# Performance work log

Hardware: AMD Instinct MI355X
Metric: run time of the kernel (lower is better)

The kernel has to match this reference:

```python
import jax, jax.numpy as jnp
import numpy as np

N = 40000      # nodes
E = 640000     # directed edges (avg degree 16)
IN_DIM = 64
HID = 64
OUT = 128
EPS_LN = 1e-5
EPS_BN = 1e-5
NEG_SLOPE = 0.2  # PyG GATConv default


def setup_inputs() -> dict:
    key = jax.random.key(0)
    ks = jax.random.split(key, 40)
    s = 0.05
    d = {}
    d["x"] = jax.random.normal(ks[0], (N, IN_DIM), jnp.float32)
    d["edge_index"] = jax.random.randint(ks[1], (2, E), 0, N, jnp.int32)
    d["pos"] = jax.random.normal(ks[2], (N, 3), jnp.float32)
    # GAT layer 1: in=64, out=64, heads=4 (concat)
    d["W1"] = jax.random.normal(ks[3], (4 * HID, IN_DIM), jnp.float32) * s
    d["a_s1"] = jax.random.normal(ks[4], (4, HID), jnp.float32) * s
    d["a_d1"] = jax.random.normal(ks[5], (4, HID), jnp.float32) * s
    d["bg1"] = jnp.zeros((4 * HID,), jnp.float32)
    d["ln1_g"] = jnp.ones((4 * HID,), jnp.float32)
    d["ln1_b"] = jnp.zeros((4 * HID,), jnp.float32)
    # GAT layer 2: in=256, out=64, heads=2 (concat)
    d["W2"] = jax.random.normal(ks[6], (2 * HID, 4 * HID), jnp.float32) * s
    d["a_s2"] = jax.random.normal(ks[7], (2, HID), jnp.float32) * s
    d["a_d2"] = jax.random.normal(ks[8], (2, HID), jnp.float32) * s
    d["bg2"] = jnp.zeros((2 * HID,), jnp.float32)
    d["ln2_g"] = jnp.ones((2 * HID,), jnp.float32)
    d["ln2_b"] = jnp.zeros((2 * HID,), jnp.float32)
    # GAT layer 3: in=128, out=128, heads=1
    d["W3"] = jax.random.normal(ks[9], (OUT, 2 * HID), jnp.float32) * s
    d["a_s3"] = jax.random.normal(ks[10], (1, OUT), jnp.float32) * s
    d["a_d3"] = jax.random.normal(ks[11], (1, OUT), jnp.float32) * s
    d["bg3"] = jnp.zeros((OUT,), jnp.float32)
    # pointnet: Conv1d(3,64,1) -> BN -> ReLU -> Conv1d(64,128,1) -> BN -> ReLU -> Conv1d(128,128,1)
    d["pw1"] = jax.random.normal(ks[12], (64, 3), jnp.float32) * s
    d["pb1"] = jnp.zeros((64,), jnp.float32)
    d["bn1_g"] = jnp.ones((64,), jnp.float32)
    d["bn1_b"] = jnp.zeros((64,), jnp.float32)
    d["pw2"] = jax.random.normal(ks[13], (128, 64), jnp.float32) * s
    d["pb2"] = jnp.zeros((128,), jnp.float32)
    d["bn2_g"] = jnp.ones((128,), jnp.float32)
    d["bn2_b"] = jnp.zeros((128,), jnp.float32)
    d["pw3"] = jax.random.normal(ks[14], (OUT, 128), jnp.float32) * s
    d["pb3"] = jnp.zeros((OUT,), jnp.float32)
    # fusion Linear(2*OUT, OUT)
    d["fw"] = jax.random.normal(ks[15], (OUT, 2 * OUT), jnp.float32) * s
    d["fb"] = jnp.zeros((OUT,), jnp.float32)
    return d


def _gat(x, W, a_s, a_d, b, src, dst, n):
    """PyG-style GATConv (concat=True, eval mode). x:[n,Fin], W:[H*C,Fin], a_*:[H,C]."""
    H, C = a_s.shape
    h = (x @ W.T).reshape(n, H, C)                       # [n,H,C]
    e_src = jnp.sum(h * a_s[None], -1)                   # [n,H]
    e_dst = jnp.sum(h * a_d[None], -1)                   # [n,H]
    e = jax.nn.leaky_relu(e_src[src] + e_dst[dst], NEG_SLOPE)   # [E,H]
    emax = jax.ops.segment_max(e, dst, num_segments=n)   # segment softmax over dst
    ex = jnp.exp(e - emax[dst])
    den = jax.ops.segment_sum(ex, dst, num_segments=n)
    alpha = ex / (den[dst] + 1e-16)                      # [E,H]
    out = jax.ops.segment_sum(alpha[:, :, None] * h[src], dst, num_segments=n)  # [n,H,C]
    return out.reshape(n, H * C) + b


def _ln(x, g, b):
    mu = jnp.mean(x, -1, keepdims=True)
    var = jnp.var(x, -1, keepdims=True)
    return (x - mu) * jax.lax.rsqrt(var + EPS_LN) * g + b


def _bn_eval(x, g, b):
    # eval-mode BatchNorm with freshly-initialized running stats (mean=0, var=1)
    return x * (g * jax.lax.rsqrt(jnp.float32(1.0 + EPS_BN))) + b


def reference(x, edge_index, pos, W1, a_s1, a_d1, bg1, ln1_g, ln1_b,
              W2, a_s2, a_d2, bg2, ln2_g, ln2_b, W3, a_s3, a_d3, bg3,
              pw1, pb1, bn1_g, bn1_b, pw2, pb2, bn2_g, bn2_b, pw3, pb3, fw, fb):
    n = x.shape[0]
    loops = jnp.arange(n, dtype=edge_index.dtype)        # PyG add_self_loops=True
    src = jnp.concatenate([edge_index[0], loops])
    dst = jnp.concatenate([edge_index[1], loops])

    x1 = jax.nn.relu(_ln(_gat(x, W1, a_s1, a_d1, bg1, src, dst, n), ln1_g, ln1_b))
    x2 = jax.nn.relu(_ln(_gat(x1, W2, a_s2, a_d2, bg2, src, dst, n), ln2_g, ln2_b))
    x3 = _gat(x2, W3, a_s3, a_d3, bg3, src, dst, n)      # [n,OUT]

    # pointnet: 1x1 conv1d == per-node linear
    p = jax.nn.relu(_bn_eval(pos @ pw1.T + pb1, bn1_g, bn1_b))
    p = jax.nn.relu(_bn_eval(p @ pw2.T + pb2, bn2_g, bn2_b))
    pos_features = p @ pw3.T + pb3                       # [n,OUT]

    combined = jnp.concatenate([x3, pos_features], -1)
    output = combined @ fw.T + fb
    return (output, x3, pos_features)
```

## Files before the change

kernel.cpp:

```cpp
#include <hip/hip_runtime.h>
#include <cstddef>

#define NNODES 40000
#define NEDGES 640000
#define NETOT  (NNODES + NEDGES)
#define ELLW   96
#define NCAST  30720
#define NBUCK  313
#define SEGCAP 8192
#define ABLOCKS 84
#define CBLOCKS 30

typedef unsigned short u16;
typedef unsigned int   u32;
using v2f = __attribute__((ext_vector_type(2))) float;

__device__ inline float wave_sum(float v) {
#pragma unroll
    for (int o = 32; o > 0; o >>= 1) v += __shfl_xor(v, o);
    return v;
}
__device__ inline u16 f2bf(float f) {
    u32 u = __float_as_uint(f);
    return (u16)((u + 0x7fffu + ((u >> 16) & 1u)) >> 16);
}

__global__ void build_a_kernel(const int* __restrict__ ei, u32* __restrict__ bcnt,
                               u32* __restrict__ seg,
                               const float* __restrict__ W1, const float* __restrict__ as1,
                               const float* __restrict__ ad1, float* __restrict__ vbuf,
                               const float* s0, u16* d0, int n0, const float* s1, u16* d1, int n1,
                               const float* s2, u16* d2, int n2, const float* s3, u16* d3, int n3,
                               const float* s4, u16* d4, int n4, const float* s5, u16* d5, int n5) {
    int tid = threadIdx.x;
    int blk = blockIdx.x;
    if (blk >= ABLOCKS) {
        if (blk < ABLOCKS + CBLOCKS) {
            int i = (blk - ABLOCKS) * 1024 + tid;
            const float* s; u16* d;
            if      (i < n0) { s = s0; d = d0; }
            else if ((i -= n0) < n1) { s = s1; d = d1; }
            else if ((i -= n1) < n2) { s = s2; d = d2; }
            else if ((i -= n2) < n3) { s = s3; d = d3; }
            else if ((i -= n3) < n4) { s = s4; d = d4; }
            else if ((i -= n4) < n5) { s = s5; d = d5; }
            else return;
            float4 v = ((const float4*)s)[i];
            ushort4 o; o.x = f2bf(v.x); o.y = f2bf(v.y); o.z = f2bf(v.z); o.w = f2bf(v.w);
            ((ushort4*)d)[i] = o;
        } else if (tid < 256) {
            int h = tid >> 6, k = tid & 63;
            float ss = 0.f, dd = 0.f;
            for (int c = 0; c < 64; c++) {
                float w = W1[(h * 64 + c) * 64 + k];
                ss += as1[h * 64 + c] * w;
                dd += ad1[h * 64 + c] * w;
            }
            vbuf[tid] = ss;
            vbuf[256 + tid] = dd;
        }
        return;
    }
    __shared__ u32 hist[NBUCK], hbase[NBUCK];
    for (int i = tid; i < NBUCK; i += 1024) hist[i] = 0;
    __syncthreads();
    u32 pk[8], loc[8]; int bj[8];
    int g0 = blk * 8192;
#pragma unroll
    for (int j = 0; j < 8; j++) {
        int g = g0 + j * 1024 + tid;
        bj[j] = -1;
        if (g < NETOT) {
            int src, dst;
            if (g < NEDGES) { src = ei[g]; dst = ei[NEDGES + g]; }
            else            { src = g - NEDGES; dst = src; }
            int b = dst >> 7;
            pk[j] = ((u32)dst << 16) | (u32)src;
            bj[j] = b;
            loc[j] = atomicAdd(&hist[b], 1u);
        }
    }
    __syncthreads();
    for (int i = tid; i < NBUCK; i += 1024) {
        u32 c = hist[i];
        hbase[i] = c ? atomicAdd(&bcnt[i], c) : 0u;
    }
    __syncthreads();
#pragma unroll
    for (int j = 0; j < 8; j++) {
        if (bj[j] >= 0) {
            u32 pos = hbase[bj[j]] + loc[j];
            if (pos < SEGCAP) seg[(size_t)bj[j] * SEGCAP + pos] = pk[j];
        }
    }
}

__global__ void build_b_kernel(const u32* __restrict__ seg, const u32* __restrict__ bcnt,
                               int* __restrict__ cnt, u16* __restrict__ srcs16,
                               int2* __restrict__ ovbuf) {
    __shared__ u32 lcnt[128];
    int tid = threadIdx.x;
    int b = blockIdx.x;
    int base = b << 7;
    if (tid < 128) lcnt[tid] = 0;
    __syncthreads();
    u32 m = bcnt[b]; if (m > SEGCAP) m = SEGCAP;
    const u32* sp = seg + (size_t)b * SEGCAP;
    for (u32 e = tid; e < m; e += 256) {
        u32 pkv = sp[e];
        u32 dst = pkv >> 16, src = pkv & 0xffffu;
        u32 p = atomicAdd(&lcnt[dst - (u32)base], 1u);
        if (p < ELLW) srcs16[dst * ELLW + p] = (u16)src;
        else {
            int q = atomicAdd(&cnt[NNODES], 1);
            ovbuf[q] = make_int2((int)dst, (int)src);
        }
    }
    __syncthreads();
    if (tid < 128 && base + tid < NNODES) cnt[base + tid] = (int)lcnt[tid];
}

__global__ void esed1_kernel(const float* __restrict__ x, const float* __restrict__ vbuf,
                             float* __restrict__ es, float* __restrict__ ed,
                             u16* __restrict__ xc) {
    __shared__ float vl[512];
    int tid = threadIdx.x;
    vl[tid] = vbuf[tid];
    vl[tid + 256] = vbuf[tid + 256];
    __syncthreads();
    int lane = tid & 63, wave = tid >> 6;
    int i = lane >> 2, q = lane & 3;
    int node = blockIdx.x * 64 + wave * 16 + i;
    const float* xp = x + (size_t)node * 64 + q * 16;
    float xr[16];
    *(float4*)&xr[0]  = ((const float4*)xp)[0];
    *(float4*)&xr[4]  = ((const float4*)xp)[1];
    *(float4*)&xr[8]  = ((const float4*)xp)[2];
    *(float4*)&xr[12] = ((const float4*)xp)[3];
    float p[8];
#pragma unroll
    for (int h = 0; h < 8; h++) {
        float s = 0.f;
#pragma unroll
        for (int j = 0; j < 16; j++) s += xr[j] * vl[h * 64 + q * 16 + j];
        p[h] = s;
    }
#pragma unroll
    for (int h = 0; h < 8; h++) {
        p[h] += __shfl_xor(p[h], 1);
        p[h] += __shfl_xor(p[h], 2);
    }
    es[node * 4 + q] = p[q];
    ed[node * 4 + q] = p[4 + q];
    u16* cp = xc + (size_t)node * 64 + q * 16;
#pragma unroll
    for (int j = 0; j < 16; j += 4) {
        ushort4 o; o.x = f2bf(xr[j]); o.y = f2bf(xr[j + 1]);
        o.z = f2bf(xr[j + 2]); o.w = f2bf(xr[j + 3]);
        *(ushort4*)(cp + j) = o;
    }
}

__global__ void gat_agg_kernel(const u16* __restrict__ xc,
                               const float* __restrict__ es, const float* __restrict__ ed,
                               const int* __restrict__ cnt, const u16* __restrict__ srcs16,
                               const int2* __restrict__ ovbuf,
                               u16* __restrict__ agg, int n) {
    __shared__ float wbuf[4][4][100];
    __shared__ u32   sbuf[4][ELLW];
    int wave = threadIdx.x >> 6;
    int wid = (blockIdx.x * blockDim.x + threadIdx.x) >> 6;
    int lane = threadIdx.x & 63;
    if (wid >= n) return;

    int degt = cnt[wid];
    int mainc = degt < ELLW ? degt : ELLW;
    int padt = (mainc + 7) & ~7;
    const u16* sp = srcs16 + (size_t)wid * ELLW;

    const int h = lane & 3;
    const int esub = lane >> 2;
    float edh = ed[(size_t)wid * 4 + h];

    float den = 0.f;
    for (int i0 = 0; i0 < padt; i0 += 16) {
        int e = i0 + esub;
        if (e < padt) {
            float w = 0.f; u32 off = 0;
            if (e < mainc) {
                int s = sp[e];
                off = (u32)s << 7;
                float v = es[(size_t)s * 4 + h] + edh;
                v = v > 0.f ? v : 0.2f * v;
                w = __expf(v);
            }
            wbuf[wave][h][e] = w;
            if (h == 0) sbuf[wave][e] = off;
            den += w;
        }
    }
    int ovn = 0;
    if (degt > ELLW) {
        ovn = cnt[n];
        for (int j = esub; j < ovn; j += 16) {
            int2 t = ovbuf[j];
            if (t.x == wid) {
                float v = es[(size_t)t.y * 4 + h] + edh;
                v = v > 0.f ? v : 0.2f * v;
                den += __expf(v);
            }
        }
    }
#pragma unroll
    for (int o = 4; o < 64; o <<= 1) den += __shfl_xor(den, o);
    float inv = 1.f / (den + 1e-16f);

    const int e2 = lane >> 5, f16 = lane & 31;
    const char* hp = (const char*)xc + f16 * 4;
    v2f a0 = {0.f, 0.f}, a1 = {0.f, 0.f}, a2 = {0.f, 0.f}, a3 = {0.f, 0.f};
    for (int eb = 0; eb < padt; eb += 8) {
        u32 of[4]; u32 g[4];
        float w0[4], w1[4], w2[4], w3[4];
#pragma unroll
        for (int k = 0; k < 4; k++) of[k] = sbuf[wave][eb + 2 * k + e2];
#pragma unroll
        for (int k = 0; k < 4; k++) g[k] = *(const u32*)(hp + of[k]);
#pragma unroll
        for (int k = 0; k < 4; k++) {
            int e = eb + 2 * k + e2;
            w0[k] = wbuf[wave][0][e]; w1[k] = wbuf[wave][1][e];
            w2[k] = wbuf[wave][2][e]; w3[k] = wbuf[wave][3][e];
        }
#pragma unroll
        for (int k = 0; k < 4; k++) {
            v2f hx;
            hx.x = __uint_as_float(g[k] << 16);
            hx.y = __uint_as_float(g[k] & 0xffff0000u);
            a0 += v2f{w0[k], w0[k]} * hx;
            a1 += v2f{w1[k], w1[k]} * hx;
            a2 += v2f{w2[k], w2[k]} * hx;
            a3 += v2f{w3[k], w3[k]} * hx;
        }
    }
    if (degt > ELLW) {
        for (int j = 0; j < ovn; j++) {
            int2 t = ovbuf[j];
            if (t.x != wid) continue;
            float wh[4];
#pragma unroll
            for (int hh = 0; hh < 4; hh++) {
                float v = es[(size_t)t.y * 4 + hh] + __shfl(edh, hh);
                v = v > 0.f ? v : 0.2f * v;
                wh[hh] = __expf(v);
            }
            if (lane < 32) {
                u32 g = *(const u32*)(hp + ((u32)t.y << 7));
                v2f hx;
                hx.x = __uint_as_float(g << 16);
                hx.y = __uint_as_float(g & 0xffff0000u);
                a0 += v2f{wh[0], wh[0]} * hx;
                a1 += v2f{wh[1], wh[1]} * hx;
                a2 += v2f{wh[2], wh[2]} * hx;
                a3 += v2f{wh[3], wh[3]} * hx;
            }
        }
    }
    a0.x += __shfl_xor(a0.x, 32); a0.y += __shfl_xor(a0.y, 32);
    a1.x += __shfl_xor(a1.x, 32); a1.y += __shfl_xor(a1.y, 32);
    a2.x += __shfl_xor(a2.x, 32); a2.y += __shfl_xor(a2.y, 32);
    a3.x += __shfl_xor(a3.x, 32); a3.y += __shfl_xor(a3.y, 32);
    float iv[4];
#pragma unroll
    for (int hh = 0; hh < 4; hh++) iv[hh] = __shfl(inv, hh);
    if (lane < 32) {
        u32* op = (u32*)agg + (size_t)wid * 128 + f16;
        op[0]  = ((u32)f2bf(a0.y * iv[0]) << 16) | f2bf(a0.x * iv[0]);
        op[32] = ((u32)f2bf(a1.y * iv[1]) << 16) | f2bf(a1.x * iv[1]);
        op[64] = ((u32)f2bf(a2.y * iv[2]) << 16) | f2bf(a2.x * iv[2]);
        op[96] = ((u32)f2bf(a3.y * iv[3]) << 16) | f2bf(a3.x * iv[3]);
    }
}

__global__ void w1ln_kernel(const u16* __restrict__ agg, const u16* __restrict__ B,
                            const float* __restrict__ bias,
                            const float* __restrict__ lng, const float* __restrict__ lnb,
                            u16* __restrict__ xb, int M) {
    using bfrag = __attribute__((ext_vector_type(8))) short;
    using ffrag = __attribute__((ext_vector_type(4))) float;
    int wave = threadIdx.x >> 6, lane = threadIdx.x & 63;
    int lm = lane & 15, kg = (lane >> 4) * 8;
    int rowblk = blockIdx.x * 64 + wave * 16;
    ffrag acc[16] = {};
#pragma unroll
    for (int hh = 0; hh < 4; hh++) {
#pragma unroll
        for (int k0 = 0; k0 < 64; k0 += 32) {
            bfrag af = *(const bfrag*)(agg + (size_t)(rowblk + lm) * 256 + hh * 64 + kg + k0);
#pragma unroll
            for (int tt = 0; tt < 4; tt++) {
                int t = hh * 4 + tt;
                bfrag bf = *(const bfrag*)(B + (size_t)(hh * 64 + tt * 16 + lm) * 64 + kg + k0);
                acc[t] = __builtin_amdgcn_mfma_f32_16x16x32_bf16(af, bf, acc[t], 0, 0, 0);
            }
        }
    }
    int orow = rowblk + (lane >> 4) * 4;
    float bi[16], gg[16], bb[16];
#pragma unroll
    for (int t = 0; t < 16; t++) {
        int col = t * 16 + lm;
        bi[t] = bias[col]; gg[t] = lng[col]; bb[t] = lnb[col];
    }
#pragma unroll
    for (int r = 0; r < 4; r++) {
        float pv[16];
        float s1 = 0.f, s2 = 0.f;
#pragma unroll
        for (int t = 0; t < 16; t++) {
            float v = acc[t][r] + bi[t];
            pv[t] = v; s1 += v; s2 += v * v;
        }
#pragma unroll
        for (int o = 1; o < 16; o <<= 1) { s1 += __shfl_xor(s1, o); s2 += __shfl_xor(s2, o); }
        float mu = s1 / 256.f;
        float var = s2 / 256.f - mu * mu;
        float rstd = rsqrtf(var + 1e-5f);
#pragma unroll
        for (int t = 0; t < 16; t++) {
            float v = (pv[t] - mu) * rstd * gg[t] + bb[t];
            v = v > 0.f ? v : 0.f;
            xb[(size_t)(orow + r) * 256 + t * 16 + lm] = f2bf(v);
        }
    }
}

template <int H, int C, bool AF32>
__global__ void gemm_scores_kernel(const void* __restrict__ Aptr, const u16* __restrict__ B,
                                   u16* __restrict__ Cout,
                                   const float* __restrict__ as, const float* __restrict__ ad,
                                   float* __restrict__ es, float* __restrict__ ed,
                                   int M, int Nn, int K) {
    constexpr int HT = 128 / C;
    using bfrag = __attribute__((ext_vector_type(8))) short;
    using ffrag = __attribute__((ext_vector_type(4))) float;
    int wave = threadIdx.x >> 6, lane = threadIdx.x & 63;
    int lm = lane & 15, kg = (lane >> 4) * 8;
    int rowblk = blockIdx.x * 64 + wave * 16;
    int n0 = blockIdx.y * 128;
    const u16* Bp = B + (size_t)(n0 + lm) * K + kg;
    ffrag acc[8] = {};
    for (int k0 = 0; k0 < K; k0 += 32) {
        bfrag af;
        if constexpr (AF32) {
            const float* ap = (const float*)Aptr + (size_t)(rowblk + lm) * K + kg + k0;
            float4 a0 = *(const float4*)ap;
            float4 a1 = *(const float4*)(ap + 4);
            af[0] = (short)f2bf(a0.x); af[1] = (short)f2bf(a0.y);
            af[2] = (short)f2bf(a0.z); af[3] = (short)f2bf(a0.w);
            af[4] = (short)f2bf(a1.x); af[5] = (short)f2bf(a1.y);
            af[6] = (short)f2bf(a1.z); af[7] = (short)f2bf(a1.w);
        } else {
            af = *(const bfrag*)((const u16*)Aptr + (size_t)(rowblk + lm) * K + kg + k0);
        }
#pragma unroll
        for (int t = 0; t < 8; t++) {
            bfrag bf = *(const bfrag*)(Bp + (size_t)t * 16 * K + k0);
            acc[t] = __builtin_amdgcn_mfma_f32_16x16x32_bf16(af, bf, acc[t], 0, 0, 0);
        }
    }
    int orow = rowblk + (lane >> 4) * 4;
    float asv[8], adv[8];
#pragma unroll
    for (int t = 0; t < 8; t++) {
        int fcol = n0 + t * 16 + lm;
        asv[t] = as[fcol]; adv[t] = ad[fcol];
    }
    float ps[4][HT] = {}, pd[4][HT] = {};
#pragma unroll
    for (int t = 0; t < 8; t++) {
        const int hh = t / (C / 16);
#pragma unroll
        for (int r = 0; r < 4; r++) {
            float v = acc[t][r];
            ps[r][hh] += v * asv[t];
            pd[r][hh] += v * adv[t];
            Cout[(size_t)(orow + r) * Nn + n0 + t * 16 + lm] = f2bf(v);
        }
    }
    int hb = blockIdx.y * HT;
#pragma unroll
    for (int r = 0; r < 4; r++)
#pragma unroll
        for (int hh = 0; hh < HT; hh++) {
            float s = ps[r][hh], d = pd[r][hh];
#pragma unroll
            for (int o = 1; o < 16; o <<= 1) { s += __shfl_xor(s, o); d += __shfl_xor(d, o); }
            if (lm == 0) {
                es[(size_t)(orow + r) * H + hb + hh] = s;
                ed[(size_t)(orow + r) * H + hb + hh] = d;
            }
        }
}

template <int H, int C, bool LNRELU>
__global__ void gat_fused_kernel(const u16* __restrict__ hmat,
                                 const float* __restrict__ es, const float* __restrict__ ed,
                                 const int* __restrict__ cnt, const u16* __restrict__ srcs16,
                                 const int2* __restrict__ ovbuf,
                                 const float* __restrict__ bias,
                                 const float* __restrict__ lng, const float* __restrict__ lnb,
                                 void* __restrict__ out, int n) {
    constexpr int HC = H * C;
    constexpr int VPT = HC / 64;
    constexpr int SH = (HC == 256) ? 9 : 8;
    constexpr int EPW = 64 / H;
    constexpr int HSH = (H == 4) ? 2 : ((H == 2) ? 1 : 0);
    __shared__ float wbuf[4][H][100];
    __shared__ int   sbuf[4][ELLW];
    int wave = threadIdx.x >> 6;
    int wid = (blockIdx.x * blockDim.x + threadIdx.x) >> 6;
    int lane = threadIdx.x & 63;
    if (wid >= n) return;

    int degt = cnt[wid];
    int mainc = degt < ELLW ? degt : ELLW;
    int pad = (mainc + 7) & ~7;
    const u16* sp = srcs16 + (size_t)wid * ELLW;

    const int h = lane & (H - 1);
    const int esub = lane >> HSH;
    float edh = ed[(size_t)wid * H + h];

    float den = 0.f;
    for (int i0 = 0; i0 < pad; i0 += EPW) {
        int e = i0 + esub;
        if (e < pad) {
            float w = 0.f;
            int soff = 0;
            if (e < mainc) {
                int s = sp[e];
                soff = s << SH;
                float v = es[(size_t)s * H + h] + edh;
                v = v > 0.f ? v : 0.2f * v;
                w = __expf(v);
            }
            wbuf[wave][h][e] = w;
            if (h == 0) sbuf[wave][e] = soff;
            den += w;
        }
    }
    int ovn = 0;
    if (degt > ELLW) {
        ovn = cnt[n];
        for (int j = esub; j < ovn; j += EPW) {
            int2 t = ovbuf[j];
            if (t.x == wid) {
                float v = es[(size_t)t.y * H + h] + edh;
                v = v > 0.f ? v : 0.2f * v;
                den += __expf(v);
            }
        }
    }
#pragma unroll
    for (int o = H; o < 64; o <<= 1) den += __shfl_xor(den, o);
    float inv = 1.f / (den + 1e-16f);

    const int myhead = (lane * VPT) / C;
    const float invh = __shfl(inv, myhead);
    const int loff = lane * (VPT * 2);
    v2f a01 = {0.f, 0.f}, a23 = {0.f, 0.f};

    for (int e = 0; e < pad; e += 8) {
        int4   o0 = *(const int4*)&sbuf[wave][e];
        int4   o1 = *(const int4*)&sbuf[wave][e + 4];
        float4 w0 = *(const float4*)&wbuf[wave][myhead][e];
        float4 w1 = *(const float4*)&wbuf[wave][myhead][e + 4];
        int   oo[8] = {o0.x, o0.y, o0.z, o0.w, o1.x, o1.y, o1.z, o1.w};
        float ww[8] = {w0.x, w0.y, w0.z, w0.w, w1.x, w1.y, w1.z, w1.w};
        if constexpr (VPT == 4) {
            uint2 gg[8];
#pragma unroll
            for (int u = 0; u < 8; u++)
                gg[u] = *(const uint2*)((const char*)hmat + (size_t)(u32)oo[u] + loff);
#pragma unroll
            for (int u = 0; u < 8; u++) {
                v2f wv = {ww[u], ww[u]};
                v2f h01, h23;
                h01.x = __uint_as_float(gg[u].x << 16);
                h01.y = __uint_as_float(gg[u].x & 0xffff0000u);
                h23.x = __uint_as_float(gg[u].y << 16);
                h23.y = __uint_as_float(gg[u].y & 0xffff0000u);
                a01 += wv * h01;
                a23 += wv * h23;
            }
        } else {
            u32 gg[8];
#pragma unroll
            for (int u = 0; u < 8; u++)
                gg[u] = *(const u32*)((const char*)hmat + (size_t)(u32)oo[u] + loff);
#pragma unroll
            for (int u = 0; u < 8; u++) {
                v2f wv = {ww[u], ww[u]};
                v2f h01;
                h01.x = __uint_as_float(gg[u] << 16);
                h01.y = __uint_as_float(gg[u] & 0xffff0000u);
                a01 += wv * h01;
            }
        }
    }
    if (degt > ELLW) {
        const float edm = __shfl(edh, myhead);
        for (int j = 0; j < ovn; j++) {
            int2 t = ovbuf[j];
            if (t.x != wid) continue;
            float v = es[(size_t)t.y * H + myhead] + edm;
            v = v > 0.f ? v : 0.2f * v;
            float w = __expf(v);
            v2f wv = {w, w};
            if constexpr (VPT == 4) {
                uint2 g = *(const uint2*)((const char*)hmat + ((size_t)t.y << SH) + loff);
                v2f h01, h23;
                h01.x = __uint_as_float(g.x << 16);
                h01.y = __uint_as_float(g.x & 0xffff0000u);
                h23.x = __uint_as_float(g.y << 16);
                h23.y = __uint_as_float(g.y & 0xffff0000u);
                a01 += wv * h01;
                a23 += wv * h23;
            } else {
                u32 g = *(const u32*)((const char*)hmat + ((size_t)t.y << SH) + loff);
                v2f h01;
                h01.x = __uint_as_float(g << 16);
                h01.y = __uint_as_float(g & 0xffff0000u);
                a01 += wv * h01;
            }
        }
    }
    {
        v2f iv = {invh, invh};
        a01 *= iv;
        a23 *= iv;
    }

    int fbase = lane * VPT;
    float y[VPT];
    y[0] = a01.x + bias[fbase + 0];
    y[1] = a01.y + bias[fbase + 1];
    if constexpr (VPT == 4) {
        y[2] = a23.x + bias[fbase + 2];
        y[3] = a23.y + bias[fbase + 3];
    }

    if constexpr (LNRELU) {
        float s1 = 0.f, s2 = 0.f;
#pragma unroll
        for (int j = 0; j < VPT; j++) { s1 += y[j]; s2 += y[j] * y[j]; }
        s1 = wave_sum(s1);
        s2 = wave_sum(s2);
        float mu = s1 / (float)HC;
        float var = s2 / (float)HC - mu * mu;
        float rstd = rsqrtf(var + 1e-5f);
#pragma unroll
        for (int j = 0; j < VPT; j++) {
            float v = (y[j] - mu) * rstd * lng[fbase + j] + lnb[fbase + j];
            y[j] = v > 0.f ? v : 0.f;
        }
        u16* op = (u16*)out + (size_t)wid * HC + fbase;
        if constexpr (VPT == 4) {
            ushort4 o; o.x = f2bf(y[0]); o.y = f2bf(y[1]); o.z = f2bf(y[2]); o.w = f2bf(y[3]);
            *(ushort4*)op = o;
        } else {
            ushort2 o; o.x = f2bf(y[0]); o.y = f2bf(y[1]);
            *(ushort2*)op = o;
        }
    } else {
        float* op = (float*)out + (size_t)wid * HC + fbase;
        if constexpr (VPT == 4) *(float4*)op = make_float4(y[0], y[1], y[2], y[3]);
        else                    *(float2*)op = make_float2(y[0], y[1]);
    }
}

__global__ void gemm_pn12_kernel(const float* __restrict__ pos,
                                 const float* __restrict__ pw1, const float* __restrict__ pb1,
                                 const float* __restrict__ bn1g, const float* __restrict__ bn1b,
                                 const u16* __restrict__ B, u16* __restrict__ Cout,
                                 const float* __restrict__ pb2,
                                 const float* __restrict__ bn2g, const float* __restrict__ bn2b,
                                 int M) {
    const int Nn = 128, K = 64;
    using bfrag = __attribute__((ext_vector_type(8))) short;
    using ffrag = __attribute__((ext_vector_type(4))) float;
    int wave = threadIdx.x >> 6, lane = threadIdx.x & 63;
    int lm = lane & 15, kg = (lane >> 4) * 8;
    int rowblk = blockIdx.x * 64 + wave * 16;
    int row = rowblk + lm;
    float p0 = pos[row * 3 + 0], p1 = pos[row * 3 + 1], p2 = pos[row * 3 + 2];
    const u16* Bp = B + (size_t)lm * K + kg;
    const float bnscale = rsqrtf(1.0f + 1e-5f);
    ffrag acc[8] = {};
#pragma unroll
    for (int k0 = 0; k0 < K; k0 += 32) {
        bfrag af;
#pragma unroll
        for (int j = 0; j < 8; j++) {
            int k = kg + k0 + j;
            float v = p0 * pw1[k * 3 + 0] + p1 * pw1[k * 3 + 1] + p2 * pw1[k * 3 + 2] + pb1[k];
            v = v * (bn1g[k] * bnscale) + bn1b[k];
            v = v > 0.f ? v : 0.f;
            af[j] = (short)f2bf(v);
        }
#pragma unroll
        for (int t = 0; t < 8; t++) {
            bfrag bf = *(const bfrag*)(Bp + (size_t)t * 16 * K + k0);
            acc[t] = __builtin_amdgcn_mfma_f32_16x16x32_bf16(af, bf, acc[t], 0, 0, 0);
        }
    }
    int orow = rowblk + (lane >> 4) * 4;
#pragma unroll
    for (int t = 0; t < 8; t++) {
        int col = t * 16 + lm;
        float bi = pb2[col], g = bn2g[col] * bnscale, bb = bn2b[col];
#pragma unroll
        for (int r = 0; r < 4; r++) {
            float v = (acc[t][r] + bi) * g + bb;
            v = v > 0.f ? v : 0.f;
            Cout[(size_t)(orow + r) * Nn + col] = f2bf(v);
        }
    }
}

__global__ void gemm_pw3cat_kernel(const u16* __restrict__ p2, const u16* __restrict__ Bpw3,
                                   const float* __restrict__ pb3, float* __restrict__ pf,
                                   const float* __restrict__ x3, const u16* __restrict__ Bfw,
                                   const float* __restrict__ fb, float* __restrict__ outp,
                                   int M) {
    using bfrag = __attribute__((ext_vector_type(8))) short;
    using ffrag = __attribute__((ext_vector_type(4))) float;
    __shared__ float pft[64][132];
    int wave = threadIdx.x >> 6, lane = threadIdx.x & 63;
    int lm = lane & 15, kg = (lane >> 4) * 8;
    int rowblk = blockIdx.x * 64 + wave * 16;

    {
        const u16* Ap = p2 + (size_t)(rowblk + lm) * 128 + kg;
        const u16* Bp = Bpw3 + (size_t)lm * 128 + kg;
        ffrag acc[8] = {};
#pragma unroll
        for (int k0 = 0; k0 < 128; k0 += 32) {
            bfrag af = *(const bfrag*)(Ap + k0);
#pragma unroll
            for (int t = 0; t < 8; t++) {
                bfrag bf = *(const bfrag*)(Bp + (size_t)t * 16 * 128 + k0);
                acc[t] = __builtin_amdgcn_mfma_f32_16x16x32_bf16(af, bf, acc[t], 0, 0, 0);
            }
        }
        int orow = rowblk + (lane >> 4) * 4;
        int lrow = wave * 16 + (lane >> 4) * 4;
#pragma unroll
        for (int t = 0; t < 8; t++) {
            int col = t * 16 + lm;
            float bi = pb3[col];
#pragma unroll
            for (int r = 0; r < 4; r++) {
                float v = acc[t][r] + bi;
                pf[(size_t)(orow + r) * 128 + col] = v;
                pft[lrow + r][col] = v;
            }
        }
    }
    __syncthreads();

    {
        const u16* Bp = Bfw + (size_t)lm * 256 + kg;
        ffrag acc[8] = {};
        int row = rowblk + lm, lrow = wave * 16 + lm;
#pragma unroll
        for (int k0 = 0; k0 < 256; k0 += 32) {
            bfrag af;
            if (k0 < 128) {
                const float* ap = x3 + (size_t)row * 128 + kg + k0;
                float4 a0 = *(const float4*)ap;
                float4 a1 = *(const float4*)(ap + 4);
                af[0] = (short)f2bf(a0.x); af[1] = (short)f2bf(a0.y);
                af[2] = (short)f2bf(a0.z); af[3] = (short)f2bf(a0.w);
                af[4] = (short)f2bf(a1.x); af[5] = (short)f2bf(a1.y);
                af[6] = (short)f2bf(a1.z); af[7] = (short)f2bf(a1.w);
            } else {
                const float* ap = &pft[lrow][kg + k0 - 128];
                float4 a0 = *(const float4*)ap;
                float4 a1 = *(const float4*)(ap + 4);
                af[0] = (short)f2bf(a0.x); af[1] = (short)f2bf(a0.y);
                af[2] = (short)f2bf(a0.z); af[3] = (short)f2bf(a0.w);
                af[4] = (short)f2bf(a1.x); af[5] = (short)f2bf(a1.y);
                af[6] = (short)f2bf(a1.z); af[7] = (short)f2bf(a1.w);
            }
#pragma unroll
            for (int t = 0; t < 8; t++) {
                bfrag bf = *(const bfrag*)(Bp + (size_t)t * 16 * 256 + k0);
                acc[t] = __builtin_amdgcn_mfma_f32_16x16x32_bf16(af, bf, acc[t], 0, 0, 0);
            }
        }
        int orow = rowblk + (lane >> 4) * 4;
#pragma unroll
        for (int t = 0; t < 8; t++) {
            int col = t * 16 + lm;
            float bi = fb[col];
#pragma unroll
            for (int r = 0; r < 4; r++)
                outp[(size_t)(orow + r) * 128 + col] = acc[t][r] + bi;
        }
    }
}

extern "C" void kernel_launch(void* const* d_in, const int* in_sizes, int n_in,
                              void* d_out, int out_size, void* d_ws, size_t ws_size,
                              hipStream_t stream) {
    const float* x    = (const float*)d_in[0];
    const int*   ei   = (const int*)d_in[1];
    const float* pos  = (const float*)d_in[2];
    const float* W1   = (const float*)d_in[3];
    const float* as1  = (const float*)d_in[4];
    const float* ad1  = (const float*)d_in[5];
    const float* bg1  = (const float*)d_in[6];
    const float* ln1g = (const float*)d_in[7];
    const float* ln1b = (const float*)d_in[8];
    const float* W2   = (const float*)d_in[9];
    const float* as2  = (const float*)d_in[10];
    const float* ad2  = (const float*)d_in[11];
    const float* bg2  = (const float*)d_in[12];
    const float* ln2g = (const float*)d_in[13];
    const float* ln2b = (const float*)d_in[14];
    const float* W3   = (const float*)d_in[15];
    const float* as3  = (const float*)d_in[16];
    const float* ad3  = (const float*)d_in[17];
    const float* bg3  = (const float*)d_in[18];
    const float* pw1  = (const float*)d_in[19];
    const float* pb1  = (const float*)d_in[20];
    const float* bn1g = (const float*)d_in[21];
    const float* bn1b = (const float*)d_in[22];
    const float* pw2  = (const float*)d_in[23];
    const float* pb2  = (const float*)d_in[24];
    const float* bn2g = (const float*)d_in[25];
    const float* bn2b = (const float*)d_in[26];
    const float* pw3  = (const float*)d_in[27];
    const float* pb3  = (const float*)d_in[28];
    const float* fw   = (const float*)d_in[29];
    const float* fb   = (const float*)d_in[30];

    const int N = NNODES;
    float* out = (float*)d_out;
    float* x3  = out + (size_t)N * 128;
    float* pf  = out + (size_t)2 * N * 128;

    char* ws = (char*)d_ws;
    size_t off = 0;
    auto alloc = [&](size_t bytes) -> void* {
        void* p = ws + off;
        off += (bytes + 255) / 256 * 256;
        return p;
    };
    int*   cnt    = (int*)alloc((size_t)(N + 1 + NBUCK) * 4);
    u32*   bcnt   = (u32*)(cnt + N + 1);
    u32*   seg    = (u32*)alloc((size_t)NBUCK * SEGCAP * 4);
    u16*   srcs16 = (u16*)alloc((size_t)N * ELLW * 2);
    int2*  ovbuf  = (int2*)alloc((size_t)NETOT * 8);
    float* esb    = (float*)alloc((size_t)N * 4 * 4);
    float* edb    = (float*)alloc((size_t)N * 4 * 4);
    u16*   w1c    = (u16*)alloc(16384 * 2);
    u16*   w2c    = (u16*)alloc(32768 * 2);
    u16*   w3c    = (u16*)alloc(16384 * 2);
    u16*   pw2c   = (u16*)alloc(8192 * 2);
    u16*   pw3c   = (u16*)alloc(16384 * 2);
    u16*   fwc    = (u16*)alloc(32768 * 2);
    u16*   hbufb  = (u16*)alloc((size_t)N * 128 * 2);
    u16*   xb     = (u16*)alloc((size_t)N * 256 * 2);
    u16*   p2b    = (u16*)alloc((size_t)N * 128 * 2);
    u16*   xc     = (u16*)alloc((size_t)N * 64 * 2);
    float* vbuf   = (float*)alloc(512 * 4);
    u16*   aggb   = (u16*)alloc((size_t)N * 256 * 2);

    hipMemsetAsync(cnt, 0, (size_t)(N + 1 + NBUCK) * 4, stream);
    build_a_kernel<<<ABLOCKS + CBLOCKS + 1, 1024, 0, stream>>>(
        ei, bcnt, seg, W1, as1, ad1, vbuf,
        W1, w1c, 4096, W2, w2c, 8192, W3, w3c, 4096,
        pw2, pw2c, 2048, pw3, pw3c, 4096, fw, fwc, 8192);
    build_b_kernel<<<NBUCK, 256, 0, stream>>>(seg, bcnt, cnt, srcs16, ovbuf);

    const int NW = N / 4;
    const int GB = N / 64;

    gemm_pn12_kernel<<<GB, 256, 0, stream>>>(
        pos, pw1, pb1, bn1g, bn1b, pw2c, p2b, pb2, bn2g, bn2b, N);

    esed1_kernel<<<GB, 256, 0, stream>>>(x, vbuf, esb, edb, xc);
    gat_agg_kernel<<<NW, 256, 0, stream>>>(xc, esb, edb, cnt, srcs16, ovbuf, aggb, N);
    w1ln_kernel<<<GB, 256, 0, stream>>>(aggb, w1c, bg1, ln1g, ln1b, xb, N);

    gemm_scores_kernel<2, 64, false><<<dim3(GB, 1), 256, 0, stream>>>(
        xb, w2c, hbufb, as2, ad2, esb, edb, N, 128, 256);
    gat_fused_kernel<2, 64, true><<<NW, 256, 0, stream>>>(
        hbufb, esb, edb, cnt, srcs16, ovbuf, bg2, ln2g, ln2b, xb, N);

    gemm_scores_kernel<1, 128, false><<<dim3(GB, 1), 256, 0, stream>>>(
        xb, w3c, hbufb, as3, ad3, esb, edb, N, 128, 128);
    gat_fused_kernel<1, 128, false><<<NW, 256, 0, stream>>>(
        hbufb, esb, edb, cnt, srcs16, ovbuf, bg3, nullptr, nullptr, x3, N);

    gemm_pw3cat_kernel<<<GB, 256, 0, stream>>>(p2b, pw3c, pb3, pf, x3, fwc, fb, out, N);
}
```

Baseline: 359.5 us.

## Fold pw3 into fusion weights so final GEMMs run as independent blocks

Precomputes M2 = fw[:,128:] @ pw3 and a combined bias (fb + fw[:,128:]@pb3) in the setup kernel. The final output is then computed directly from p2 and x3 without waiting on pos_features. This splits the final kernel into two independent block types: one writes pf and one writes out. That removes the LDS staging and __syncthreads dependency and doubles the grid for more parallelism. The cost is extra setup blocks, plus a slightly different rounding path because the product matrix is rounded to bf16.

```diff
diff --git a/kernel.cpp b/kernel.cpp
--- a/kernel.cpp
+++ b/kernel.cpp
@@ -10,6 +10,7 @@
 #define SEGCAP 8192
 #define ABLOCKS 84
 #define CBLOCKS 30
+#define ACB (ABLOCKS + CBLOCKS)
 
 typedef unsigned short u16;
 typedef unsigned int   u32;
@@ -29,13 +30,16 @@
                                u32* __restrict__ seg,
                                const float* __restrict__ W1, const float* __restrict__ as1,
                                const float* __restrict__ ad1, float* __restrict__ vbuf,
+                               const float* __restrict__ pw3, const float* __restrict__ pb3,
+                               const float* __restrict__ fw, const float* __restrict__ fb,
+                               u16* __restrict__ m2c, float* __restrict__ cvb,
                                const float* s0, u16* d0, int n0, const float* s1, u16* d1, int n1,
                                const float* s2, u16* d2, int n2, const float* s3, u16* d3, int n3,
                                const float* s4, u16* d4, int n4, const float* s5, u16* d5, int n5) {
     int tid = threadIdx.x;
     int blk = blockIdx.x;
     if (blk >= ABLOCKS) {
-        if (blk < ABLOCKS + CBLOCKS) {
+        if (blk < ACB) {
             int i = (blk - ABLOCKS) * 1024 + tid;
             const float* s; u16* d;
             if      (i < n0) { s = s0; d = d0; }
@@ -48,16 +52,32 @@
             float4 v = ((const float4*)s)[i];
             ushort4 o; o.x = f2bf(v.x); o.y = f2bf(v.y); o.z = f2bf(v.z); o.w = f2bf(v.w);
             ((ushort4*)d)[i] = o;
-        } else if (tid < 256) {
-            int h = tid >> 6, k = tid & 63;
-            float ss = 0.f, dd = 0.f;
-            for (int c = 0; c < 64; c++) {
-                float w = W1[(h * 64 + c) * 64 + k];
-                ss += as1[h * 64 + c] * w;
-                dd += ad1[h * 64 + c] * w;
-            }
-            vbuf[tid] = ss;
-            vbuf[256 + tid] = dd;
+        } else if (blk == ACB) {
+            if (tid < 256) {
+                int h = tid >> 6, k = tid & 63;
+                float ss = 0.f, dd = 0.f;
+                for (int c = 0; c < 64; c++) {
+                    float w = W1[(h * 64 + c) * 64 + k];
+                    ss += as1[h * 64 + c] * w;
+                    dd += ad1[h * 64 + c] * w;
+                }
+                vbuf[tid] = ss;
+                vbuf[256 + tid] = dd;
+            }
+        } else if (blk < ACB + 17) {
+            int entry = (blk - (ACB + 1)) * 1024 + tid;
+            int o = entry >> 7, k = entry & 127;
+            float s = 0.f;
+            for (int j = 0; j < 128; j++)
+                s += fw[o * 256 + 128 + j] * pw3[j * 128 + k];
+            m2c[o * 128 + k] = f2bf(s);
+        } else {
+            if (tid < 128) {
+                float s = fb[tid];
+                for (int j = 0; j < 128; j++)
+                    s += fw[tid * 256 + 128 + j] * pb3[j];
+                cvb[tid] = s;
+            }
         }
         return;
     }
@@ -628,22 +648,21 @@
     }
 }
 
-__global__ void gemm_pw3cat_kernel(const u16* __restrict__ p2, const u16* __restrict__ Bpw3,
-                                   const float* __restrict__ pb3, float* __restrict__ pf,
-                                   const float* __restrict__ x3, const u16* __restrict__ Bfw,
-                                   const float* __restrict__ fb, float* __restrict__ outp,
-                                   int M) {
+__global__ void gemm_final_kernel(const u16* __restrict__ p2, const u16* __restrict__ pw3c,
+                                  const float* __restrict__ pb3, float* __restrict__ pf,
+                                  const float* __restrict__ x3, const u16* __restrict__ fwc,
+                                  const u16* __restrict__ m2c, const float* __restrict__ cvb,
+                                  float* __restrict__ outp, int M) {
     using bfrag = __attribute__((ext_vector_type(8))) short;
     using ffrag = __attribute__((ext_vector_type(4))) float;
-    __shared__ float pft[64][132];
     int wave = threadIdx.x >> 6, lane = threadIdx.x & 63;
     int lm = lane & 15, kg = (lane >> 4) * 8;
-    int rowblk = blockIdx.x * 64 + wave * 16;
-
-    {
+    int task = blockIdx.x & 1;
+    int rowblk = (blockIdx.x >> 1) * 64 + wave * 16;
+    ffrag acc[8] = {};
+    if (task) {
         const u16* Ap = p2 + (size_t)(rowblk + lm) * 128 + kg;
-        const u16* Bp = Bpw3 + (size_t)lm * 128 + kg;
-        ffrag acc[8] = {};
+        const u16* Bp = pw3c + (size_t)lm * 128 + kg;
 #pragma unroll
         for (int k0 = 0; k0 < 128; k0 += 32) {
             bfrag af = *(const bfrag*)(Ap + k0);
@@ -654,48 +673,41 @@
             }
         }
         int orow = rowblk + (lane >> 4) * 4;
-        int lrow = wave * 16 + (lane >> 4) * 4;
 #pragma unroll
         for (int t = 0; t < 8; t++) {
             int col = t * 16 + lm;
             float bi = pb3[col];
 #pragma unroll
-            for (int r = 0; r < 4; r++) {
-                float v = acc[t][r] + bi;
-                pf[(size_t)(orow + r) * 128 + col] = v;
-                pft[lrow + r][col] = v;
-            }
-        }
-    }
-    __syncthreads();
-
-    {
-        const u16* Bp = Bfw + (size_t)lm * 256 + kg;
-        ffrag acc[8] = {};
-        int row = rowblk + lm, lrow = wave * 16 + lm;
-#pragma unroll
-        for (int k0 = 0; k0 < 256; k0 += 32) {
+            for (int r = 0; r < 4; r++)
+                pf[(size_t)(orow + r) * 128 + col] = acc[t][r] + bi;
+        }
+    } else {
+        int row = rowblk + lm;
+        const u16* Bp1 = fwc + (size_t)lm * 256 + kg;
+#pragma unroll
+        for (int k0 = 0; k0 < 128; k0 += 32) {
+            const float* ap = x3 + (size_t)row * 128 + kg + k0;
+            float4 a0 = *(const float4*)ap;
+            float4 a1 = *(const float4*)(ap + 4);
             bfrag af;
-            if (k0 < 128) {
-                const float* ap = x3 + (size_t)row * 128 + kg + k0;
-                float4 a0 = *(const float4*)ap;
-                float4 a1 = *(const float4*)(ap + 4);
-                af[0] = (short)f2bf(a0.x); af[1] = (short)f2bf(a0.y);
-                af[2] = (short)f2bf(a0.z); af[3] = (short)f2bf(a0.w);
-                af[4] = (short)f2bf(a1.x); af[5] = (short)f2bf(a1.y);
-                af[6] = (short)f2bf(a1.z); af[7] = (short)f2bf(a1.w);
-            } else {
-                const float* ap = &pft[lrow][kg + k0 - 128];
-                float4 a0 = *(const float4*)ap;
-                float4 a1 = *(const float4*)(ap + 4);
-                af[0] = (short)f2bf(a0.x); af[1] = (short)f2bf(a0.y);
-                af[2] = (short)f2bf(a0.z); af[3] = (short)f2bf(a0.w);
-                af[4] = (short)f2bf(a1.x); af[5] = (short)f2bf(a1.y);
-                af[6] = (short)f2bf(a1.z); af[7] = (short)f2bf(a1.w);
-            }
+            af[0] = (short)f2bf(a0.x); af[1] = (short)f2bf(a0.y);
+            af[2] = (short)f2bf(a0.z); af[3] = (short)f2bf(a0.w);
+            af[4] = (short)f2bf(a1.x); af[5] = (short)f2bf(a1.y);
+            af[6] = (short)f2bf(a1.z); af[7] = (short)f2bf(a1.w);
 #pragma unroll
             for (int t = 0; t < 8; t++) {
-                bfrag bf = *(const bfrag*)(Bp + (size_t)t * 16 * 256 + k0);
+                bfrag bf = *(const bfrag*)(Bp1 + (size_t)t * 16 * 256 + k0);
+                acc[t] = __builtin_amdgcn_mfma_f32_16x16x32_bf16(af, bf, acc[t], 0, 0, 0);
+            }
+        }
+        const u16* Ap2 = p2 + (size_t)row * 128 + kg;
+        const u16* Bp2 = m2c + (size_t)lm * 128 + kg;
+#pragma unroll
+        for (int k0 = 0; k0 < 128; k0 += 32) {
+            bfrag af = *(const bfrag*)(Ap2 + k0);
+#pragma unroll
+            for (int t = 0; t < 8; t++) {
+                bfrag bf = *(const bfrag*)(Bp2 + (size_t)t * 16 * 128 + k0);
                 acc[t] = __builtin_amdgcn_mfma_f32_16x16x32_bf16(af, bf, acc[t], 0, 0, 0);
             }
         }
@@ -703,7 +715,7 @@
 #pragma unroll
         for (int t = 0; t < 8; t++) {
             int col = t * 16 + lm;
-            float bi = fb[col];
+            float bi = cvb[col];
 #pragma unroll
             for (int r = 0; r < 4; r++)
                 outp[(size_t)(orow + r) * 128 + col] = acc[t][r] + bi;
@@ -771,6 +783,8 @@
     u16*   pw2c   = (u16*)alloc(8192 * 2);
     u16*   pw3c   = (u16*)alloc(16384 * 2);
     u16*   fwc    = (u16*)alloc(32768 * 2);
+    u16*   m2c    = (u16*)alloc(16384 * 2);
+    float* cvb    = (float*)alloc(128 * 4);
     u16*   hbufb  = (u16*)alloc((size_t)N * 128 * 2);
     u16*   xb     = (u16*)alloc((size_t)N * 256 * 2);
     u16*   p2b    = (u16*)alloc((size_t)N * 128 * 2);
@@ -779,8 +793,8 @@
     u16*   aggb   = (u16*)alloc((size_t)N * 256 * 2);
 
     hipMemsetAsync(cnt, 0, (size_t)(N + 1 + NBUCK) * 4, stream);
-    build_a_kernel<<<ABLOCKS + CBLOCKS + 1, 1024, 0, stream>>>(
-        ei, bcnt, seg, W1, as1, ad1, vbuf,
+    build_a_kernel<<<ACB + 18, 1024, 0, stream>>>(
+        ei, bcnt, seg, W1, as1, ad1, vbuf, pw3, pb3, fw, fb, m2c, cvb,
         W1, w1c, 4096, W2, w2c, 8192, W3, w3c, 4096,
         pw2, pw2c, 2048, pw3, pw3c, 4096, fw, fwc, 8192);
     build_b_kernel<<<NBUCK, 256, 0, stream>>>(seg, bcnt, cnt, srcs16, ovbuf);
@@ -805,5 +819,6 @@
     gat_fused_kernel<1, 128, false><<<NW, 256, 0, stream>>>(
         hbufb, esb, edb, cnt, srcs16, ovbuf, bg3, nullptr, nullptr, x3, N);
 
-    gemm_pw3cat_kernel<<<GB, 256, 0, stream>>>(p2b, pw3c, pb3, pf, x3, fwc, fb, out, N);
-}
+    gemm_final_kernel<<<2 * GB, 256, 0, stream>>>(
+        p2b, pw3c, pb3, pf, x3, fwc, m2c, cvb, out, N);
+}
```

Result: slower. 369.4 us (+2.8%).
